# Kernel optimization log

Hardware: AMD Instinct MI355X
Metric: run time of the kernel (lower is better)

Reference implementation:

```python
import jax, jax.numpy as jnp
import numpy as np

B, E, H, KVH, S = 1, 4096, 32, 8, 2048
HD = E // H            # per-head dim = 128
KVE = KVH * HD         # kv projection embed dim = 1024


def setup_inputs() -> dict:
    key = jax.random.key(0)
    ks = jax.random.split(key, 10)
    std = 0.02
    return {
        "input_embeds": jax.random.normal(ks[0], (B, E, 1, S), jnp.float32),
        "cos": jax.random.uniform(ks[1], (HD, S), jnp.float32, -1.0, 1.0),
        "sin": jax.random.uniform(ks[2], (HD, S), jnp.float32, -1.0, 1.0),
        "wq": jax.random.normal(ks[3], (E, E), jnp.float32) * std,
        "bq": jnp.zeros((E,), jnp.float32),
        "wk": jax.random.normal(ks[4], (KVE, E), jnp.float32) * std,
        "wv": jax.random.normal(ks[5], (KVE, E), jnp.float32) * std,
        "bv": jnp.zeros((KVE,), jnp.float32),
        "wo": jax.random.normal(ks[6], (E, E), jnp.float32) * std,
        "bo": jnp.zeros((E,), jnp.float32),
    }


def _proj(w, x, b=None):
    # 1x1 Conv2d == channelwise linear on (B, C, 1, S)
    y = jnp.einsum('oc,bcxs->boxs', w, x)
    if b is not None:
        y = y + b[None, :, None, None]
    return y


def _rope(x, cos, sin):
    # x: (B, h, HD, S); rotate-half along head_dim axis
    half = x.shape[2] // 2
    x1, x2 = x[:, :, :half], x[:, :, half:]
    rot = jnp.concatenate([-x2, x1], axis=2)
    return x * cos[None, None] + rot * sin[None, None]


def reference(input_embeds, cos, sin, wq, bq, wk, wv, bv, wo, bo):
    b, e, _, s = input_embeds.shape
    hd = e // H
    q = _proj(wq, input_embeds, bq)          # (B, E, 1, S)
    k = _proj(wk, input_embeds)              # (B, KVE, 1, S)  (no bias)
    v = _proj(wv, input_embeds, bv)          # (B, KVE, 1, S)

    qh = q.reshape(b, H, hd, s)
    kh = k.reshape(b, KVH, hd, s)
    qh = _rope(qh, cos, sin)
    kh = _rope(kh, cos, sin)

    # GQA tiling: channel-block repeat => query head h uses kv head (h % KVH)
    rep = H // KVH
    kfull = jnp.tile(kh, (1, rep, 1, 1))                       # (B, H, HD, S)
    vfull = jnp.tile(v.reshape(b, KVH, hd, s), (1, rep, 1, 1))  # (B, H, HD, S)

    scale = 1.0 / np.sqrt(hd).astype(np.float32)
    scores = jnp.einsum('bhcq,bhck->bhqk', qh, kfull) * scale  # (B, H, S, S)
    causal = jnp.tril(jnp.ones((s, s), bool))
    scores = jnp.where(causal[None, None], scores, jnp.finfo(scores.dtype).min)
    w = jax.nn.softmax(scores, axis=-1)
    attn = jnp.einsum('bhqk,bhck->bhcq', w, vfull).reshape(b, e, 1, s)
    return _proj(wo, attn, bo)
```

## Files before the change

### kernel.cpp

```cpp
#include <hip/hip_runtime.h>


typedef unsigned short u16;
typedef unsigned int u32;
typedef __attribute__((ext_vector_type(8))) short bf16x8;
typedef __attribute__((ext_vector_type(4))) float f32x4;

__device__ __forceinline__ u16 f2b(float f){
  union { float f; u32 u; } v; v.f = f;
  u32 r = (v.u + 0x7FFFu + ((v.u >> 16) & 1u)) >> 16;
  return (u16)r;
}
__device__ __forceinline__ float b2f(u16 b){
  union { u32 u; float f; } v; v.u = ((u32)b) << 16;
  return v.f;
}

__device__ __forceinline__ void gld16(const void* g, void* l){
  __builtin_amdgcn_global_load_lds((const __attribute__((address_space(1))) u32*)g,
                                   (__attribute__((address_space(3))) u32*)l, 16, 0, 0);
}

__global__ __launch_bounds__(256) void cvt_w(const float* __restrict__ src,
                                             u16* __restrict__ dst, int n4)
{
  int i = blockIdx.x * 256 + threadIdx.x;
  if (i < n4){
    float4 v = *(const float4*)&src[(size_t)i * 4];
    ushort4 o; o.x = f2b(v.x); o.y = f2b(v.y); o.z = f2b(v.z); o.w = f2b(v.w);
    *(ushort4*)&dst[(size_t)i * 4] = o;
  }
}

__global__ __launch_bounds__(256) void transpose_x(const float* __restrict__ X,
                                                   u16* __restrict__ XT)
{
  __shared__ float lds[64][65];
  const int c0 = blockIdx.x * 64, s0 = blockIdx.y * 64;
  const int tid = threadIdx.x;
  {
    const int sg = tid & 15, cl = tid >> 4;
#pragma unroll
    for (int p = 0; p < 4; ++p){
      int c = cl + p * 16;
      float4 v = *(const float4*)&X[(size_t)(c0 + c) * 2048 + s0 + sg * 4];
      lds[sg*4+0][c] = v.x; lds[sg*4+1][c] = v.y;
      lds[sg*4+2][c] = v.z; lds[sg*4+3][c] = v.w;
    }
  }
  __syncthreads();
  {
    const int cg = tid & 15, sl = tid >> 4;
#pragma unroll
    for (int p = 0; p < 4; ++p){
      int s = sl + p * 16;
      ushort4 o;
      o.x = f2b(lds[s][cg*4+0]); o.y = f2b(lds[s][cg*4+1]);
      o.z = f2b(lds[s][cg*4+2]); o.w = f2b(lds[s][cg*4+3]);
      *(ushort4*)&XT[(size_t)(s0 + s) * 4096 + c0 + cg * 4] = o;
    }
  }
}

template<int EPI, int ABF>
__global__ __launch_bounds__(256) void gemm2(
    const u16* __restrict__ W0, const u16* __restrict__ W1, const u16* __restrict__ W2,
    const float* __restrict__ F0, const float* __restrict__ F1, const float* __restrict__ F2,
    const u16* __restrict__ B,
    const float* __restrict__ bias0, const float* __restrict__ bias2,
    u16* __restrict__ QTo, u16* __restrict__ KTo, u16* __restrict__ Vno,
    float* __restrict__ OUT)
{
  const int K = 4096;
  const int m0 = blockIdx.y * 128, n0 = blockIdx.x * 128;

  const u16* A16; const float* Af; int mA;
  if (EPI == 0){
    if (m0 < 4096)      { A16 = W0; Af = F0; mA = m0; }
    else if (m0 < 5120) { A16 = W1; Af = F1; mA = m0 - 4096; }
    else                { A16 = W2; Af = F2; mA = m0 - 5120; }
  } else { A16 = W0; Af = F0; mA = m0; }

  __shared__ __align__(16) u16 As[128 * 32];
  __shared__ __align__(16) u16 Bs[128 * 32];

  const int tid = threadIdx.x, lane = tid & 63, w = tid >> 6;
  const int wm = w >> 1, wn = w & 1, quad = lane >> 4, l15 = lane & 15;

  f32x4 acc[4][4];
#pragma unroll
  for (int mt = 0; mt < 4; ++mt)
#pragma unroll
    for (int nt = 0; nt < 4; ++nt)
      acc[mt][nt] = f32x4{0.f, 0.f, 0.f, 0.f};

  const int r0 = tid >> 2, gs0 = tid & 3;
  const int g0 = gs0 ^ ((r0 >> 1) & 3);
  const int r1 = r0 + 64;

  u16* ldsA0 = As + (size_t)(w * 64) * 8;
  u16* ldsA1 = As + (size_t)(w * 64 + 256) * 8;
  u16* ldsB0 = Bs + (size_t)(w * 64) * 8;
  u16* ldsB1 = Bs + (size_t)(w * 64 + 256) * 8;

  const u16* bsrc0 = &B[(size_t)(n0 + r0) * 4096 + g0 * 8];
  const u16* bsrc1 = &B[(size_t)(n0 + r1) * 4096 + g0 * 8];
  const u16* asrc0 = ABF ? &A16[(size_t)(mA + r0) * 4096 + g0 * 8] : nullptr;
  const u16* asrc1 = ABF ? &A16[(size_t)(mA + r1) * 4096 + g0 * 8] : nullptr;
  const float* afs0 = ABF ? nullptr : &Af[(size_t)(mA + r0) * 4096 + g0 * 8];
  const float* afs1 = ABF ? nullptr : &Af[(size_t)(mA + r1) * 4096 + g0 * 8];

  int aoff[4], boff[4];
#pragma unroll
  for (int mt = 0; mt < 4; ++mt){
    int row = wm * 64 + mt * 16 + l15;
    aoff[mt] = row * 32 + (quad ^ ((row >> 1) & 3)) * 8;
  }
#pragma unroll
  for (int nt = 0; nt < 4; ++nt){
    int row = wn * 64 + nt * 16 + l15;
    boff[nt] = row * 32 + (quad ^ ((row >> 1) & 3)) * 8;
  }

  for (int kt = 0; kt < K / 32; ++kt){
    const int k0 = kt * 32;
    if (ABF){
      gld16(asrc0 + k0, ldsA0);
      gld16(asrc1 + k0, ldsA1);
    } else {
      float4 v0 = *(const float4*)&afs0[k0];
      float4 v1 = *(const float4*)&afs0[k0 + 4];
      float4 v2 = *(const float4*)&afs1[k0];
      float4 v3 = *(const float4*)&afs1[k0 + 4];
      union { u16 u[8]; uint4 q; } p0, p1;
      p0.u[0]=f2b(v0.x); p0.u[1]=f2b(v0.y); p0.u[2]=f2b(v0.z); p0.u[3]=f2b(v0.w);
      p0.u[4]=f2b(v1.x); p0.u[5]=f2b(v1.y); p0.u[6]=f2b(v1.z); p0.u[7]=f2b(v1.w);
      p1.u[0]=f2b(v2.x); p1.u[1]=f2b(v2.y); p1.u[2]=f2b(v2.z); p1.u[3]=f2b(v2.w);
      p1.u[4]=f2b(v3.x); p1.u[5]=f2b(v3.y); p1.u[6]=f2b(v3.z); p1.u[7]=f2b(v3.w);
      *(uint4*)&As[(size_t)tid * 8] = p0.q;
      *(uint4*)&As[(size_t)(tid + 256) * 8] = p1.q;
    }
    gld16(bsrc0 + k0, ldsB0);
    gld16(bsrc1 + k0, ldsB1);
    __syncthreads();

    bf16x8 af[4], bfr[4];
#pragma unroll
    for (int mt = 0; mt < 4; ++mt) af[mt]  = *(const bf16x8*)&As[aoff[mt]];
#pragma unroll
    for (int nt = 0; nt < 4; ++nt) bfr[nt] = *(const bf16x8*)&Bs[boff[nt]];
#pragma unroll
    for (int mt = 0; mt < 4; ++mt)
#pragma unroll
      for (int nt = 0; nt < 4; ++nt)
        acc[mt][nt] = __builtin_amdgcn_mfma_f32_16x16x32_bf16(af[mt], bfr[nt], acc[mt][nt], 0, 0, 0);
    __syncthreads();
  }

  if (EPI == 0){
    if (m0 < 4096){
#pragma unroll
      for (int mt = 0; mt < 4; ++mt){
        int mb = m0 + wm * 64 + mt * 16 + quad * 4;
        float b0 = bias0[mb], b1 = bias0[mb+1], b2 = bias0[mb+2], b3 = bias0[mb+3];
#pragma unroll
        for (int nt = 0; nt < 4; ++nt){
          int n = n0 + wn * 64 + nt * 16 + l15;
          ushort4 o;
          o.x = f2b(acc[mt][nt][0] + b0); o.y = f2b(acc[mt][nt][1] + b1);
          o.z = f2b(acc[mt][nt][2] + b2); o.w = f2b(acc[mt][nt][3] + b3);
          *(ushort4*)&QTo[(size_t)n * 4096 + mb] = o;
        }
      }
    } else if (m0 < 5120){
#pragma unroll
      for (int mt = 0; mt < 4; ++mt){
        int mb = m0 - 4096 + wm * 64 + mt * 16 + quad * 4;
#pragma unroll
        for (int nt = 0; nt < 4; ++nt){
          int n = n0 + wn * 64 + nt * 16 + l15;
          ushort4 o;
          o.x = f2b(acc[mt][nt][0]); o.y = f2b(acc[mt][nt][1]);
          o.z = f2b(acc[mt][nt][2]); o.w = f2b(acc[mt][nt][3]);
          *(ushort4*)&KTo[(size_t)n * 1024 + mb] = o;
        }
      }
    } else {
#pragma unroll
      for (int mt = 0; mt < 4; ++mt)
#pragma unroll
        for (int r = 0; r < 4; ++r){
          int mv = m0 - 5120 + wm * 64 + mt * 16 + quad * 4 + r;
          float bb = bias2[mv];
#pragma unroll
          for (int nt = 0; nt < 4; ++nt){
            int n = n0 + wn * 64 + nt * 16 + l15;
            Vno[(size_t)mv * 2048 + n] = f2b(acc[mt][nt][r] + bb);
          }
        }
    }
  } else {
#pragma unroll
    for (int mt = 0; mt < 4; ++mt)
#pragma unroll
      for (int r = 0; r < 4; ++r){
        int m = m0 + wm * 64 + mt * 16 + quad * 4 + r;
        float bb = bias0[m];
#pragma unroll
        for (int nt = 0; nt < 4; ++nt){
          int n = n0 + wn * 64 + nt * 16 + l15;
          OUT[(size_t)m * 2048 + n] = acc[mt][nt][r] + bb;
        }
      }
  }
}

__global__ __launch_bounds__(256) void rope_kernel(u16* __restrict__ QT,
                                                   u16* __restrict__ KT,
                                                   const float* __restrict__ cosp,
                                                   const float* __restrict__ sinp)
{
  const float qscale = 0.08838834764831845f * 1.4426950408889634f;
  int gid = blockIdx.x * 256 + threadIdx.x;
  const int NQ = 2048 * 32 * 64;
  if (gid < NQ){
    int c = gid & 63, hh = (gid >> 6) & 31, s = gid >> 11;
    size_t base = (size_t)s * 4096 + hh * 128 + c;
    float x1 = b2f(QT[base]), x2 = b2f(QT[base + 64]);
    float c1 = cosp[c * 2048 + s],        s1 = sinp[c * 2048 + s];
    float c2 = cosp[(c + 64) * 2048 + s], s2 = sinp[(c + 64) * 2048 + s];
    QT[base]      = f2b((x1 * c1 - x2 * s1) * qscale);
    QT[base + 64] = f2b((x2 * c2 + x1 * s2) * qscale);
  } else {
    int g = gid - NQ;
    int c = g & 63, hh = (g >> 6) & 7, s = g >> 9;
    size_t base = (size_t)s * 1024 + hh * 128 + c;
    float x1 = b2f(KT[base]), x2 = b2f(KT[base + 64]);
    float c1 = cosp[c * 2048 + s],        s1 = sinp[c * 2048 + s];
    float c2 = cosp[(c + 64) * 2048 + s], s2 = sinp[(c + 64) * 2048 + s];
    KT[base]      = f2b(x1 * c1 - x2 * s1);
    KT[base + 64] = f2b(x2 * c2 + x1 * s2);
  }
}

__global__ __launch_bounds__(256, 2) void attn2(const u16* __restrict__ QT,
                                                const u16* __restrict__ KT,
                                                const u16* __restrict__ Vn,
                                                u16* __restrict__ AT)
{
  const int hg = blockIdx.x;
  const int t  = 63 - (int)blockIdx.y;
  const int w  = threadIdx.x >> 6;
  const int h  = hg * 4 + w;
  const int kvh = h & 7;
  const int lane = threadIdx.x & 63;
  const int quad = lane >> 4, l15 = lane & 15;
  const int i0 = t * 32;
  const int niter = (t >> 1) + 1;

  __shared__ __align__(16) u16 Ps[4][32][72];

  bf16x8 qa[2][4];
#pragma unroll
  for (int mt = 0; mt < 2; ++mt)
#pragma unroll
    for (int kc = 0; kc < 4; ++kc)
      qa[mt][kc] = *(const bf16x8*)&QT[(size_t)(i0 + mt * 16 + l15) * 4096
                                       + h * 128 + kc * 32 + quad * 8];

  f32x4 oacc[2][9];
#pragma unroll
  for (int mt = 0; mt < 2; ++mt)
#pragma unroll
    for (int ct = 0; ct < 9; ++ct)
      oacc[mt][ct] = f32x4{0.f, 0.f, 0.f, 0.f};

  bf16x8 ones;
#pragma unroll
  for (int z = 0; z < 8; ++z) ones[z] = (short)0x3F80;

  for (int it = 0; it < niter; ++it){
    const int j0 = it * 64;

    bf16x8 kb[4][4];
#pragma unroll
    for (int nt = 0; nt < 4; ++nt)
#pragma unroll
      for (int kc = 0; kc < 4; ++kc)
        kb[nt][kc] = *(const bf16x8*)&KT[(size_t)(j0 + nt * 16 + l15) * 1024
                                         + kvh * 128 + kc * 32 + quad * 8];
    f32x4 sacc[2][4];
#pragma unroll
    for (int mt = 0; mt < 2; ++mt)
#pragma unroll
      for (int nt = 0; nt < 4; ++nt)
        sacc[mt][nt] = f32x4{0.f, 0.f, 0.f, 0.f};
#pragma unroll
    for (int nt = 0; nt < 4; ++nt)
#pragma unroll
      for (int kc = 0; kc < 4; ++kc){
        sacc[0][nt] = __builtin_amdgcn_mfma_f32_16x16x32_bf16(qa[0][kc], kb[nt][kc], sacc[0][nt], 0, 0, 0);
        sacc[1][nt] = __builtin_amdgcn_mfma_f32_16x16x32_bf16(qa[1][kc], kb[nt][kc], sacc[1][nt], 0, 0, 0);
      }

    const bool maskit = (it == niter - 1);
#pragma unroll
    for (int mt = 0; mt < 2; ++mt)
#pragma unroll
      for (int nt = 0; nt < 4; ++nt)
#pragma unroll
        for (int r = 0; r < 4; ++r){
          float p = exp2f(fminf(sacc[mt][nt][r], 60.0f));
          if (maskit && (j0 + nt * 16 + l15 > i0 + mt * 16 + quad * 4 + r)) p = 0.0f;
          Ps[w][mt * 16 + quad * 4 + r][nt * 16 + l15] = f2b(p);
        }

    bf16x8 pa[2][2];
#pragma unroll
    for (int mt = 0; mt < 2; ++mt)
#pragma unroll
      for (int kc = 0; kc < 2; ++kc)
        pa[mt][kc] = *(const bf16x8*)&Ps[w][mt * 16 + l15][kc * 32 + quad * 8];

#pragma unroll
    for (int ct = 0; ct < 8; ++ct)
#pragma unroll
      for (int kc = 0; kc < 2; ++kc){
        bf16x8 vb = *(const bf16x8*)&Vn[(size_t)(kvh * 128 + ct * 16 + l15) * 2048
                                        + j0 + kc * 32 + quad * 8];
        oacc[0][ct] = __builtin_amdgcn_mfma_f32_16x16x32_bf16(pa[0][kc], vb, oacc[0][ct], 0, 0, 0);
        oacc[1][ct] = __builtin_amdgcn_mfma_f32_16x16x32_bf16(pa[1][kc], vb, oacc[1][ct], 0, 0, 0);
      }
#pragma unroll
    for (int kc = 0; kc < 2; ++kc){
      oacc[0][8] = __builtin_amdgcn_mfma_f32_16x16x32_bf16(pa[0][kc], ones, oacc[0][8], 0, 0, 0);
      oacc[1][8] = __builtin_amdgcn_mfma_f32_16x16x32_bf16(pa[1][kc], ones, oacc[1][8], 0, 0, 0);
    }
  }

#pragma unroll
  for (int mt = 0; mt < 2; ++mt){
    float rinv[4];
#pragma unroll
    for (int r = 0; r < 4; ++r) rinv[r] = 1.0f / oacc[mt][8][r];
#pragma unroll
    for (int ct = 0; ct < 8; ++ct)
#pragma unroll
      for (int r = 0; r < 4; ++r){
        int i = i0 + mt * 16 + quad * 4 + r;
        int c = ct * 16 + l15;
        AT[(size_t)i * 4096 + h * 128 + c] = f2b(oacc[mt][ct][r] * rinv[r]);
      }
  }
}

extern "C" void kernel_launch(void* const* d_in, const int* in_sizes, int n_in,
                              void* d_out, int out_size, void* d_ws, size_t ws_size,
                              hipStream_t stream)
{
  const float* X    = (const float*)d_in[0];
  const float* cosp = (const float*)d_in[1];
  const float* sinp = (const float*)d_in[2];
  const float* wq   = (const float*)d_in[3];
  const float* bq   = (const float*)d_in[4];
  const float* wk   = (const float*)d_in[5];
  const float* wv   = (const float*)d_in[6];
  const float* bv   = (const float*)d_in[7];
  const float* wo   = (const float*)d_in[8];
  const float* bo   = (const float*)d_in[9];
  float* out = (float*)d_out;

  char* ws = (char*)d_ws;
  const size_t MB = 1u << 20;

  if (ws_size >= 88 * MB){
    u16* W16Q = (u16*)(ws);
    u16* W16K = (u16*)(ws + 32 * MB);
    u16* W16V = (u16*)(ws + 40 * MB);
    u16* XT   = (u16*)(ws + 48 * MB);
    u16* QT   = (u16*)(ws + 64 * MB);
    u16* KT   = (u16*)(ws + 80 * MB);
    u16* Vn   = (u16*)(ws + 84 * MB);
    u16* AT   = (u16*)(ws + 48 * MB);
    u16* WO16 = (u16*)(ws);

    cvt_w<<<16384, 256, 0, stream>>>(wq, W16Q, 4194304);
    cvt_w<<< 4096, 256, 0, stream>>>(wk, W16K, 1048576);
    cvt_w<<< 4096, 256, 0, stream>>>(wv, W16V, 1048576);
    transpose_x<<<dim3(64, 32), 256, 0, stream>>>(X, XT);
    gemm2<0,1><<<dim3(16, 48), 256, 0, stream>>>(W16Q, W16K, W16V, wq, wk, wv,
                                                 XT, bq, bv, QT, KT, Vn, nullptr);
    cvt_w<<<16384, 256, 0, stream>>>(wo, WO16, 4194304);
    rope_kernel<<<20480, 256, 0, stream>>>(QT, KT, cosp, sinp);
    attn2<<<dim3(8, 64), 256, 0, stream>>>(QT, KT, Vn, AT);
    gemm2<1,1><<<dim3(16, 32), 256, 0, stream>>>(WO16, nullptr, nullptr, wo, nullptr, nullptr,
                                                 AT, bo, nullptr, nullptr, nullptr, nullptr, out);
  } else {
    u16* XT = (u16*)(ws);
    u16* QT = (u16*)(ws + 16 * MB);
    u16* KT = (u16*)(ws + 32 * MB);
    u16* Vn = (u16*)(ws + 36 * MB);
    u16* AT = (u16*)(ws + 40 * MB);

    transpose_x<<<dim3(64, 32), 256, 0, stream>>>(X, XT);
    gemm2<0,0><<<dim3(16, 48), 256, 0, stream>>>(nullptr, nullptr, nullptr, wq, wk, wv,
                                                 XT, bq, bv, QT, KT, Vn, nullptr);
    rope_kernel<<<20480, 256, 0, stream>>>(QT, KT, cosp, sinp);
    attn2<<<dim3(8, 64), 256, 0, stream>>>(QT, KT, Vn, AT);
    gemm2<1,0><<<dim3(16, 32), 256, 0, stream>>>(nullptr, nullptr, nullptr, wo, nullptr, nullptr,
                                                 AT, bo, nullptr, nullptr, nullptr, nullptr, out);
  }
}
```

Measured before the change: 687.2 us.

## Restructure attention: one head per block, paired causal tiles, LDS-staged K/V

The attention kernel now gives each block a single query head. Each wave handles two query tiles paired from opposite ends of the causal triangle (k and 63-k), which balances work across waves and blocks. K and V tiles are staged into swizzled shared memory with async global-to-LDS loads (K double-buffered), so all four waves share each K/V fetch instead of each wave reading them from global memory separately. This adds __syncthreads barriers, doubles register pressure (two accumulator sets, launch bounds of 1 block per CU), and drops the grid to 256 blocks, which may reduce occupancy.

```diff
diff --git a/kernel.cpp b/kernel.cpp
--- a/kernel.cpp
+++ b/kernel.cpp
@@ -243,114 +243,173 @@
   }
 }
 
-__global__ __launch_bounds__(256, 2) void attn2(const u16* __restrict__ QT,
+__global__ __launch_bounds__(256, 1) void attn3(const u16* __restrict__ QT,
                                                 const u16* __restrict__ KT,
                                                 const u16* __restrict__ Vn,
                                                 u16* __restrict__ AT)
 {
-  const int hg = blockIdx.x;
-  const int t  = 63 - (int)blockIdx.y;
-  const int w  = threadIdx.x >> 6;
-  const int h  = hg * 4 + w;
+  const int h = blockIdx.x;
+  const int p = blockIdx.y;
   const int kvh = h & 7;
-  const int lane = threadIdx.x & 63;
+  const int tid = threadIdx.x;
+  const int w = tid >> 6, lane = tid & 63;
   const int quad = lane >> 4, l15 = lane & 15;
-  const int i0 = t * 32;
-  const int niter = (t >> 1) + 1;
-
-  __shared__ __align__(16) u16 Ps[4][32][72];
-
-  bf16x8 qa[2][4];
+
+  const int k  = 4 * p + w;
+  const int t1 = k, t2 = 63 - k;
+  const int e1 = t1 >> 1, e2 = t2 >> 1;
+  const int i01 = t1 * 32, i02 = t2 * 32;
+  const int U = 32 - 2 * p;
+
+  __shared__ __align__(16) u16 Ks[2][64 * 128];
+  __shared__ __align__(16) u16 Vs[128 * 64];
+  __shared__ __align__(16) u16 Ps[4][16][64];
+
+  bf16x8 qa1[2][4], qa2[2][4];
 #pragma unroll
   for (int mt = 0; mt < 2; ++mt)
 #pragma unroll
-    for (int kc = 0; kc < 4; ++kc)
-      qa[mt][kc] = *(const bf16x8*)&QT[(size_t)(i0 + mt * 16 + l15) * 4096
-                                       + h * 128 + kc * 32 + quad * 8];
-
-  f32x4 oacc[2][9];
+    for (int kc = 0; kc < 4; ++kc){
+      qa1[mt][kc] = *(const bf16x8*)&QT[(size_t)(i01 + mt * 16 + l15) * 4096
+                                        + h * 128 + kc * 32 + quad * 8];
+      qa2[mt][kc] = *(const bf16x8*)&QT[(size_t)(i02 + mt * 16 + l15) * 4096
+                                        + h * 128 + kc * 32 + quad * 8];
+    }
+
+  f32x4 o1[2][9], o2[2][9];
 #pragma unroll
   for (int mt = 0; mt < 2; ++mt)
 #pragma unroll
-    for (int ct = 0; ct < 9; ++ct)
-      oacc[mt][ct] = f32x4{0.f, 0.f, 0.f, 0.f};
+    for (int ct = 0; ct < 9; ++ct){
+      o1[mt][ct] = f32x4{0.f, 0.f, 0.f, 0.f};
+      o2[mt][ct] = f32x4{0.f, 0.f, 0.f, 0.f};
+    }
 
   bf16x8 ones;
 #pragma unroll
   for (int z = 0; z < 8; ++z) ones[z] = (short)0x3F80;
 
-  for (int it = 0; it < niter; ++it){
-    const int j0 = it * 64;
-
-    bf16x8 kb[4][4];
-#pragma unroll
-    for (int nt = 0; nt < 4; ++nt)
-#pragma unroll
-      for (int kc = 0; kc < 4; ++kc)
-        kb[nt][kc] = *(const bf16x8*)&KT[(size_t)(j0 + nt * 16 + l15) * 1024
-                                         + kvh * 128 + kc * 32 + quad * 8];
-    f32x4 sacc[2][4];
-#pragma unroll
-    for (int mt = 0; mt < 2; ++mt)
+  const int krl = lane >> 4, kgl = lane & 15;
+  const int vrl = lane >> 3, vgl = lane & 7;
+
+  auto stageK = [&](int buf, int j0){
+#pragma unroll
+    for (int q = 0; q < 4; ++q){
+      int r = w * 16 + q * 4 + krl;
+      gld16(&KT[(size_t)(j0 + r) * 1024 + kvh * 128 + ((kgl ^ (r & 7)) * 8)],
+            &Ks[buf][(size_t)(w * 16 + q * 4) * 128]);
+    }
+  };
+  auto stageV = [&](int j0){
+#pragma unroll
+    for (int q = 0; q < 4; ++q){
+      int r = w * 32 + q * 8 + vrl;
+      gld16(&Vn[(size_t)(kvh * 128 + r) * 2048 + j0 + ((vgl ^ (r & 7)) * 8)],
+            &Vs[(size_t)(w * 32 + q * 8) * 64]);
+    }
+  };
+
+  auto soft = [&](f32x4 (&s)[2][4], bf16x8 (&pa)[2][2], f32x4 (&o)[2][9],
+                  int i0, int j0, bool maskit){
+#pragma unroll
+    for (int mt = 0; mt < 2; ++mt){
 #pragma unroll
       for (int nt = 0; nt < 4; ++nt)
-        sacc[mt][nt] = f32x4{0.f, 0.f, 0.f, 0.f};
-#pragma unroll
-    for (int nt = 0; nt < 4; ++nt)
-#pragma unroll
-      for (int kc = 0; kc < 4; ++kc){
-        sacc[0][nt] = __builtin_amdgcn_mfma_f32_16x16x32_bf16(qa[0][kc], kb[nt][kc], sacc[0][nt], 0, 0, 0);
-        sacc[1][nt] = __builtin_amdgcn_mfma_f32_16x16x32_bf16(qa[1][kc], kb[nt][kc], sacc[1][nt], 0, 0, 0);
+#pragma unroll
+        for (int r = 0; r < 4; ++r){
+          float pv = exp2f(fminf(s[mt][nt][r], 60.0f));
+          if (maskit && (j0 + nt * 16 + l15 > i0 + mt * 16 + quad * 4 + r)) pv = 0.0f;
+          int col = nt * 16 + l15, rowp = quad * 4 + r;
+          Ps[w][rowp][((col >> 3) ^ (rowp & 7)) * 8 + (col & 7)] = f2b(pv);
+        }
+#pragma unroll
+      for (int kc = 0; kc < 2; ++kc){
+        pa[mt][kc] = *(const bf16x8*)&Ps[w][l15][((kc * 4 + quad) ^ (l15 & 7)) * 8];
+        o[mt][8] = __builtin_amdgcn_mfma_f32_16x16x32_bf16(pa[mt][kc], ones, o[mt][8], 0, 0, 0);
       }
-
-    const bool maskit = (it == niter - 1);
-#pragma unroll
-    for (int mt = 0; mt < 2; ++mt)
-#pragma unroll
-      for (int nt = 0; nt < 4; ++nt)
+    }
+  };
+
+  auto epilogue = [&](f32x4 (&o)[2][9], int i0){
+#pragma unroll
+    for (int mt = 0; mt < 2; ++mt){
+      float rinv[4];
+#pragma unroll
+      for (int r = 0; r < 4; ++r) rinv[r] = 1.0f / o[mt][8][r];
+#pragma unroll
+      for (int ct = 0; ct < 8; ++ct)
 #pragma unroll
         for (int r = 0; r < 4; ++r){
-          float p = exp2f(fminf(sacc[mt][nt][r], 60.0f));
-          if (maskit && (j0 + nt * 16 + l15 > i0 + mt * 16 + quad * 4 + r)) p = 0.0f;
-          Ps[w][mt * 16 + quad * 4 + r][nt * 16 + l15] = f2b(p);
-        }
-
-    bf16x8 pa[2][2];
-#pragma unroll
-    for (int mt = 0; mt < 2; ++mt)
-#pragma unroll
-      for (int kc = 0; kc < 2; ++kc)
-        pa[mt][kc] = *(const bf16x8*)&Ps[w][mt * 16 + l15][kc * 32 + quad * 8];
-
-#pragma unroll
-    for (int ct = 0; ct < 8; ++ct)
-#pragma unroll
-      for (int kc = 0; kc < 2; ++kc){
-        bf16x8 vb = *(const bf16x8*)&Vn[(size_t)(kvh * 128 + ct * 16 + l15) * 2048
-                                        + j0 + kc * 32 + quad * 8];
-        oacc[0][ct] = __builtin_amdgcn_mfma_f32_16x16x32_bf16(pa[0][kc], vb, oacc[0][ct], 0, 0, 0);
-        oacc[1][ct] = __builtin_amdgcn_mfma_f32_16x16x32_bf16(pa[1][kc], vb, oacc[1][ct], 0, 0, 0);
+          int i = i0 + mt * 16 + quad * 4 + r;
+          AT[(size_t)i * 4096 + h * 128 + ct * 16 + l15] = f2b(o[mt][ct][r] * rinv[r]);
+        }
+    }
+  };
+
+  stageK(0, 0);
+  for (int u = 0; u < U; ++u){
+    __syncthreads();
+    if (u + 1 < U) stageK((u + 1) & 1, (u + 1) * 64);
+    stageV(u * 64);
+
+    const int j0 = u * 64;
+    const bool act1 = (u <= e1), act2 = (u <= e2);
+    const u16* Kb = &Ks[u & 1][0];
+
+    f32x4 s1[2][4], s2[2][4];
+    bf16x8 pa1[2][2], pa2[2][2];
+    if (act2 || act1){
+#pragma unroll
+      for (int mt = 0; mt < 2; ++mt)
+#pragma unroll
+        for (int nt = 0; nt < 4; ++nt){
+          s1[mt][nt] = f32x4{0.f, 0.f, 0.f, 0.f};
+          s2[mt][nt] = f32x4{0.f, 0.f, 0.f, 0.f};
+        }
+#pragma unroll
+      for (int nt = 0; nt < 4; ++nt){
+        bf16x8 kb[4];
+#pragma unroll
+        for (int kc = 0; kc < 4; ++kc){
+          int row = nt * 16 + l15;
+          kb[kc] = *(const bf16x8*)&Kb[row * 128 + (((kc * 4 + quad) ^ (row & 7)) * 8)];
+        }
+#pragma unroll
+        for (int kc = 0; kc < 4; ++kc){
+          s2[0][nt] = __builtin_amdgcn_mfma_f32_16x16x32_bf16(qa2[0][kc], kb[kc], s2[0][nt], 0, 0, 0);
+          s2[1][nt] = __builtin_amdgcn_mfma_f32_16x16x32_bf16(qa2[1][kc], kb[kc], s2[1][nt], 0, 0, 0);
+        }
+        if (act1)
+#pragma unroll
+          for (int kc = 0; kc < 4; ++kc){
+            s1[0][nt] = __builtin_amdgcn_mfma_f32_16x16x32_bf16(qa1[0][kc], kb[kc], s1[0][nt], 0, 0, 0);
+            s1[1][nt] = __builtin_amdgcn_mfma_f32_16x16x32_bf16(qa1[1][kc], kb[kc], s1[1][nt], 0, 0, 0);
+          }
       }
-#pragma unroll
-    for (int kc = 0; kc < 2; ++kc){
-      oacc[0][8] = __builtin_amdgcn_mfma_f32_16x16x32_bf16(pa[0][kc], ones, oacc[0][8], 0, 0, 0);
-      oacc[1][8] = __builtin_amdgcn_mfma_f32_16x16x32_bf16(pa[1][kc], ones, oacc[1][8], 0, 0, 0);
-    }
-  }
-
-#pragma unroll
-  for (int mt = 0; mt < 2; ++mt){
-    float rinv[4];
-#pragma unroll
-    for (int r = 0; r < 4; ++r) rinv[r] = 1.0f / oacc[mt][8][r];
-#pragma unroll
-    for (int ct = 0; ct < 8; ++ct)
-#pragma unroll
-      for (int r = 0; r < 4; ++r){
-        int i = i0 + mt * 16 + quad * 4 + r;
-        int c = ct * 16 + l15;
-        AT[(size_t)i * 4096 + h * 128 + c] = f2b(oacc[mt][ct][r] * rinv[r]);
-      }
+      if (act2) soft(s2, pa2, o2, i02, j0, u == e2);
+      if (act1) soft(s1, pa1, o1, i01, j0, u == e1);
+    }
+    __syncthreads();
+
+    if (act2 || act1){
+#pragma unroll
+      for (int ct = 0; ct < 8; ++ct)
+#pragma unroll
+        for (int kc = 0; kc < 2; ++kc){
+          int row = ct * 16 + l15;
+          bf16x8 vb = *(const bf16x8*)&Vs[row * 64 + (((kc * 4 + quad) ^ (row & 7)) * 8)];
+          if (act2){
+            o2[0][ct] = __builtin_amdgcn_mfma_f32_16x16x32_bf16(pa2[0][kc], vb, o2[0][ct], 0, 0, 0);
+            o2[1][ct] = __builtin_amdgcn_mfma_f32_16x16x32_bf16(pa2[1][kc], vb, o2[1][ct], 0, 0, 0);
+          }
+          if (act1){
+            o1[0][ct] = __builtin_amdgcn_mfma_f32_16x16x32_bf16(pa1[0][kc], vb, o1[0][ct], 0, 0, 0);
+            o1[1][ct] = __builtin_amdgcn_mfma_f32_16x16x32_bf16(pa1[1][kc], vb, o1[1][ct], 0, 0, 0);
+          }
+        }
+      if (u == e2) epilogue(o2, i02);
+      if (u == e1) epilogue(o1, i01);
+    }
   }
 }
 
@@ -392,7 +451,7 @@
                                                  XT, bq, bv, QT, KT, Vn, nullptr);
     cvt_w<<<16384, 256, 0, stream>>>(wo, WO16, 4194304);
     rope_kernel<<<20480, 256, 0, stream>>>(QT, KT, cosp, sinp);
-    attn2<<<dim3(8, 64), 256, 0, stream>>>(QT, KT, Vn, AT);
+    attn3<<<dim3(32, 8), 256, 0, stream>>>(QT, KT, Vn, AT);
     gemm2<1,1><<<dim3(16, 32), 256, 0, stream>>>(WO16, nullptr, nullptr, wo, nullptr, nullptr,
                                                  AT, bo, nullptr, nullptr, nullptr, nullptr, out);
   } else {
@@ -406,7 +465,7 @@
     gemm2<0,0><<<dim3(16, 48), 256, 0, stream>>>(nullptr, nullptr, nullptr, wq, wk, wv,
                                                  XT, bq, bv, QT, KT, Vn, nullptr);
     rope_kernel<<<20480, 256, 0, stream>>>(QT, KT, cosp, sinp);
-    attn2<<<dim3(8, 64), 256, 0, stream>>>(QT, KT, Vn, AT);
+    attn3<<<dim3(32, 8), 256, 0, stream>>>(QT, KT, Vn, AT);
     gemm2<1,0><<<dim3(16, 32), 256, 0, stream>>>(nullptr, nullptr, nullptr, wo, nullptr, nullptr,
                                                  AT, bo, nullptr, nullptr, nullptr, nullptr, out);
   }
```

Result: faster. 662.0 us (-3.7%).
